# Kernel optimization log

Measured on AMD Instinct MI355X. Metric: run time of the kernel, lower is better.

## Reference

```python
import jax, jax.numpy as jnp
import numpy as np

B, N, C = 16, 2048, 128
NCLS = 40


def setup_inputs() -> dict:
    key = jax.random.key(0)
    ks = iter(jax.random.split(key, 40))

    def nrm(shape, s=0.05):
        return jax.random.normal(next(ks), shape, dtype=jnp.float32) * s

    return {
        "x": jax.random.normal(next(ks), (B, 3, N), dtype=jnp.float32),
        "conv1_w": nrm((128, 3), 0.5),
        "bn1_g": jnp.ones((128,), jnp.float32), "bn1_b": jnp.zeros((128,), jnp.float32),
        "conv2_w": nrm((128, 128)),
        "bn2_g": jnp.ones((128,), jnp.float32), "bn2_b": jnp.zeros((128,), jnp.float32),
        "sa_wqk": nrm((4, 32, 128)),
        "sa_wv": nrm((4, 128, 128)), "sa_bv": nrm((4, 128)),
        "sa_wt": nrm((4, 128, 128)), "sa_bt": nrm((4, 128)),
        "sa_g": jnp.ones((4, 128), jnp.float32), "sa_b": jnp.zeros((4, 128), jnp.float32),
        "fuse_w": nrm((1024, 512)),
        "fuse_g": jnp.ones((1024,), jnp.float32), "fuse_b": jnp.zeros((1024,), jnp.float32),
        "lin1_w": nrm((512, 1024)),
        "bn6_g": jnp.ones((512,), jnp.float32), "bn6_b": jnp.zeros((512,), jnp.float32),
        "lin2_w": nrm((256, 512)), "lin2_b": jnp.zeros((256,), jnp.float32),
        "bn7_g": jnp.ones((256,), jnp.float32), "bn7_b": jnp.zeros((256,), jnp.float32),
        "lin3_w": nrm((NCLS, 256)), "lin3_b": jnp.zeros((NCLS,), jnp.float32),
    }


def _pconv(w, x):
    # 1x1 Conv1d == channel matmul: [O,C] x [B,C,N] -> [B,O,N]
    return jnp.einsum('oc,bcn->bon', w, x)


def _fwd(x, conv1_w, bn1_g, bn1_b, conv2_w, bn2_g, bn2_b,
         sa_wqk, sa_wv, sa_bv, sa_wt, sa_bt, sa_g, sa_b,
         fuse_w, fuse_g, fuse_b, lin1_w, bn6_g, bn6_b,
         lin2_w, lin2_b, bn7_g, bn7_b, lin3_w, lin3_b):
    # conv stem (BN in eval mode: running mean=0, var=1 -> affine)
    h = jax.nn.relu(bn1_g[:, None] * _pconv(conv1_w, x) + bn1_b[:, None])
    h = jax.nn.relu(bn2_g[:, None] * _pconv(conv2_w, h) + bn2_b[:, None])

    outs = []
    for i in range(4):  # fixed number of structurally identical SA blocks
        # q_conv and k_conv share the same weight (aliased in the torch code)
        q = jnp.einsum('dc,bcn->bdn', sa_wqk[i], h)           # [B,32,N]
        energy = jnp.einsum('bdi,bdj->bij', q, q)             # [B,N,N]
        att = jax.nn.softmax(energy, axis=-1)
        att = att / (1e-9 + att.sum(axis=1, keepdims=True))   # extra L1 renorm over dim=1
        v = _pconv(sa_wv[i], h) + sa_bv[i][:, None]           # [B,C,N]
        x_r = jnp.einsum('bcn,bnm->bcm', v, att)              # [B,C,N]
        t = _pconv(sa_wt[i], h - x_r) + sa_bt[i][:, None]
        h = h + jax.nn.relu(sa_g[i][:, None] * t + sa_b[i][:, None])
        outs.append(h)

    cat = jnp.concatenate(outs, axis=1)                        # [B,512,N]
    f = fuse_g[:, None] * _pconv(fuse_w, cat) + fuse_b[:, None]
    f = jnp.where(f > 0, f, 0.2 * f)                           # LeakyReLU(0.2)
    g = f.max(axis=-1)                                         # adaptive max pool -> [B,1024]

    h1 = jax.nn.relu(bn6_g * (g @ lin1_w.T) + bn6_b)           # dropout = identity (eval)
    h2 = jax.nn.relu(bn7_g * (h1 @ lin2_w.T + lin2_b) + bn7_b)
    return h2 @ lin3_w.T + lin3_b                              # [B,40]


def reference(x, conv1_w, bn1_g, bn1_b, conv2_w, bn2_g, bn2_b,
              sa_wqk, sa_wv, sa_bv, sa_wt, sa_bt, sa_g, sa_b,
              fuse_w, fuse_g, fuse_b, lin1_w, bn6_g, bn6_b,
              lin2_w, lin2_b, bn7_g, bn7_b, lin3_w, lin3_b):
    return _fwd(x, conv1_w, bn1_g, bn1_b, conv2_w, bn2_g, bn2_b,
                sa_wqk, sa_wv, sa_bv, sa_wt, sa_bt, sa_g, sa_b,
                fuse_w, fuse_g, fuse_b, lin1_w, bn6_g, bn6_b,
                lin2_w, lin2_b, bn7_g, bn7_b, lin3_w, lin3_b)
```

## Files before the change

### kernel.cpp

```cpp
#include <hip/hip_runtime.h>

typedef __attribute__((ext_vector_type(4))) float f4;
typedef __attribute__((ext_vector_type(8))) short s16x8;
typedef __attribute__((ext_vector_type(4))) unsigned short us4;
typedef __attribute__((ext_vector_type(2))) unsigned int u32x2;
typedef unsigned short u16;
typedef unsigned int u32;

#define DEVI __device__ __forceinline__

DEVI u16 f2bf(float f){
    u32 u = __builtin_bit_cast(u32, f);
    u32 r = (u + 0x7fffu + ((u >> 16) & 1u)) >> 16;
    return (u16)r;
}
DEVI f4 mfma16(s16x8 a, s16x8 b, f4 c){
    return __builtin_amdgcn_mfma_f32_16x16x32_bf16(a, b, c, 0, 0, 0);
}
DEVI u32 cvtpk(float lo, float hi){
    u32 r;
    asm("v_cvt_pk_bf16_f32 %0, %1, %2" : "=v"(r) : "v"(lo), "v"(hi));
    return r;
}
DEVI void gload(const u16* g, u16* l){
    __builtin_amdgcn_global_load_lds((const __attribute__((address_space(1))) void*)g,
                                     (__attribute__((address_space(3))) void*)l, 16, 0, 0);
}

#define L2E 1.44269504088896340736f

__global__ __launch_bounds__(256) void k_cast(const float* w2, const float* wqk,
                                              const float* wv, const float* wt,
                                              const float* wf, u16* out){
    int i = blockIdx.x * 256 + threadIdx.x;
    if(i < 16384)       out[i] = f2bf(w2[i]);
    else if(i < 32768)  out[i] = f2bf(wqk[i - 16384]);
    else if(i < 98304)  out[i] = f2bf(wv[i - 32768]);
    else if(i < 163840) out[i] = f2bf(wt[i - 98304]);
    else if(i < 688128){
        int t = i - 163840;
        int o = t >> 9, c = t & 511;
        int jg = o >> 4, l15 = o & 15, ks = c >> 5, kr = c & 31;
        out[163840 + (size_t)(jg*16 + ks)*512 + l15*32 + kr] = f2bf(wf[t]);
    }
}

__global__ __launch_bounds__(256) void k_stem1(const float* x, const float* w1,
                                               const float* g1, const float* b1, u16* h1tb){
    int t = blockIdx.x * 256 + threadIdx.x;
    int b = t >> 11, n = t & 2047;
    const float* xb = x + (size_t)b * 3 * 2048 + n;
    float x0 = xb[0], x1 = xb[2048], x2 = xb[4096];
    u32* o = (u32*)(h1tb + (size_t)t * 128);
    #pragma unroll 8
    for(int c = 0; c < 128; c += 2){
        float a0 = fmaxf(g1[c]   * (w1[c*3+0]*x0 + w1[c*3+1]*x1 + w1[c*3+2]*x2) + b1[c],   0.f);
        float a1 = fmaxf(g1[c+1] * (w1[c*3+3]*x0 + w1[c*3+4]*x1 + w1[c*3+5]*x2) + b1[c+1], 0.f);
        o[c >> 1] = (u32)f2bf(a0) | ((u32)f2bf(a1) << 16);
    }
}

DEVI int swz512(int bid){ return ((bid & 7) << 6) | (bid >> 3); }
DEVI int swz1024(int bid){ return ((bid & 7) << 7) | (bid >> 3); }

DEVI void qv_phase(const u16* T, const u16* wqkb, const u16* wvb, const float* bv,
                   u16* qb, u16* vt, int b, int n0, int wv_, int l15, int kg){
    f4 accv[8], accq[2];
    #pragma unroll
    for(int j=0;j<8;j++) accv[j] = (f4){0.f,0.f,0.f,0.f};
    accq[0] = (f4){0.f,0.f,0.f,0.f}; accq[1] = accq[0];
    int row = wv_*16 + l15;
    #pragma unroll
    for(int ks=0; ks<4; ks++){
        s16x8 a = *(const s16x8*)&T[row*128 + ((ks*32 + kg*8) ^ ((row&7)<<3))];
        #pragma unroll
        for(int j=0;j<8;j++){
            s16x8 bb = *(const s16x8*)(wvb + (size_t)(j*16 + l15)*128 + ks*32 + kg*8);
            accv[j] = mfma16(a, bb, accv[j]);
        }
        #pragma unroll
        for(int f=0; f<2; f++){
            s16x8 wf_ = *(const s16x8*)(wqkb + (size_t)(f*16 + l15)*128 + ks*32 + kg*8);
            accq[f] = mfma16(wf_, a, accq[f]);
        }
    }
    int nb = n0 + wv_*16;
    int it = nb >> 5;
    int k0 = (nb & 31) + kg*4;
    int vbase = ((k0 >> 3)*16)*8 + (k0 & 7);
    #pragma unroll
    for(int j=0;j<8;j++){
        float bvo = bv[j*16 + l15];
        us4 pk;
        #pragma unroll
        for(int r=0;r<4;r++) pk[r] = f2bf(accv[j][r] + bvo);
        *(us4*)(vt + (size_t)((b*64 + it)*8 + j)*512 + vbase + l15*8) = pk;
    }
    int n = n0 + wv_*16 + l15;
    #pragma unroll
    for(int f=0; f<2; f++){
        us4 pk;
        #pragma unroll
        for(int r=0;r<4;r++) pk[r] = f2bf(accq[f][r]);
        *(us4*)(qb + (size_t)(b*2048 + n)*32 + f*16 + kg*4) = pk;
    }
}

__global__ __launch_bounds__(256) void k_conv2qv(const u16* h1tb, const u16* w2b,
                                                 const float* g2, const float* b2,
                                                 float* ht0,
                                                 const u16* wqkb, const u16* wvb,
                                                 const float* bv, u16* qb, u16* vt){
    __shared__ u16 T[8192];
    int bid2 = swz512(blockIdx.x);
    int b = bid2 >> 5;
    int n0 = (bid2 & 31) << 6;
    int lane = threadIdx.x & 63, wv_ = threadIdx.x >> 6;
    int l15 = lane & 15, kg = lane >> 4;
    const u16* arow = h1tb + (size_t)(b*2048 + n0 + wv_*16 + l15) * 128 + kg*8;
    f4 acc[8];
    #pragma unroll
    for(int j=0;j<8;j++) acc[j] = (f4){0.f,0.f,0.f,0.f};
    #pragma unroll
    for(int ks=0; ks<4; ks++){
        s16x8 a = *(const s16x8*)(arow + ks*32);
        #pragma unroll
        for(int j=0;j<8;j++){
            s16x8 bb = *(const s16x8*)(w2b + (size_t)(j*16 + l15)*128 + ks*32 + kg*8);
            acc[j] = mfma16(a, bb, acc[j]);
        }
    }
    int nn0 = n0 + wv_*16 + kg*4;
    #pragma unroll
    for(int j=0;j<8;j++){
        int o = j*16 + l15;
        float gg = g2[o], be = b2[o];
        #pragma unroll
        for(int r=0;r<4;r++){
            float h = fmaxf(gg * acc[j][r] + be, 0.f);
            int nl = wv_*16 + kg*4 + r;
            ht0[(size_t)(b*2048 + nn0 + r) * 128 + o] = h;
            T[nl*128 + (o ^ ((nl&7)<<3))] = f2bf(h);
        }
    }
    __syncthreads();
    qv_phase(T, wqkb, wvb, bv, qb, vt, b, n0, wv_, l15, kg);
}

__global__ __launch_bounds__(256) void k_passA(const u16* qb, float* crowp){
    int bid2 = swz1024(blockIdx.x);
    int b = bid2 >> 6;
    int rest = bid2 & 63;
    int i0 = (rest >> 1) << 6;
    int jh = rest & 1;
    int jbeg = jh << 10;
    int lane = threadIdx.x & 63, wv_ = threadIdx.x >> 6;
    int l15 = lane & 15, kg = lane >> 4;
    const u16* qbase = qb + (size_t)b * 2048 * 32;
    s16x8 af = *(const s16x8*)(qbase + (size_t)(i0 + wv_*16 + l15)*32 + kg*8);
    float m[4], s[4], mml[4];
    const f4 z = {0.f,0.f,0.f,0.f};
    {
        s16x8 b0 = *(const s16x8*)(qbase + (size_t)(jbeg + l15)*32 + kg*8);
        s16x8 b1 = *(const s16x8*)(qbase + (size_t)(jbeg + 16 + l15)*32 + kg*8);
        f4 e0 = mfma16(af, b0, z);
        f4 e1 = mfma16(af, b1, z);
        #pragma unroll
        for(int r=0;r<4;r++){
            m[r] = fmaxf(e0[r], e1[r]);
            mml[r] = -m[r]*L2E;
            s[r] = exp2f(fmaf(e0[r], L2E, mml[r])) + exp2f(fmaf(e1[r], L2E, mml[r]));
        }
    }
    for(int j0=jbeg+32; j0<jbeg+1024; j0+=32){
        s16x8 b0 = *(const s16x8*)(qbase + (size_t)(j0 + l15)*32 + kg*8);
        s16x8 b1 = *(const s16x8*)(qbase + (size_t)(j0 + 16 + l15)*32 + kg*8);
        f4 e0 = mfma16(af, b0, z);
        f4 e1 = mfma16(af, b1, z);
        #pragma unroll
        for(int r=0;r<4;r++){
            float mx = fmaxf(e0[r], e1[r]);
            if(mx > m[r] + 8.f){
                s[r] *= exp2f((m[r]-mx)*L2E);
                m[r] = mx; mml[r] = -mx*L2E;
            }
            s[r] += exp2f(fmaf(e0[r], L2E, mml[r])) + exp2f(fmaf(e1[r], L2E, mml[r]));
        }
    }
    #pragma unroll
    for(int d=1; d<16; d<<=1){
        #pragma unroll
        for(int r=0;r<4;r++){
            float mo = __shfl_xor(m[r], d);
            float so = __shfl_xor(s[r], d);
            float mn = fmaxf(m[r], mo);
            s[r] = s[r]*exp2f((m[r]-mn)*L2E) + so*exp2f((mo-mn)*L2E);
            m[r] = mn;
        }
    }
    if(l15 == 0){
        #pragma unroll
        for(int r=0;r<4;r++){
            int i = i0 + wv_*16 + kg*4 + r;
            crowp[jh*32768 + b*2048 + i] = m[r]*L2E + log2f(s[r]);
        }
    }
}

__global__ __launch_bounds__(256) void k_passB(const u16* qb, const u16* vt,
                                               const float* crowp,
                                               const float* hprev, int ldh,
                                               u16* dtb){
    __shared__ u16 V[2][8192];
    __shared__ u16 P[2][4096];
    __shared__ float CR[2048];
    __shared__ float csl[64];
    int bid2 = swz512(blockIdx.x);
    int b = bid2 >> 5;
    int j0 = (bid2 & 31) << 6;
    int tid = threadIdx.x;
    int lane = tid & 63, wv_ = tid >> 6;
    int l15 = lane & 15, kg = lane >> 4;
    int jh = wv_ * 16;
    const u16* qbase = qb + (size_t)b * 2048 * 32;
    const u16* vtb = vt + (size_t)b * 64*8*512;

    #pragma unroll
    for(int p=0;p<8;p++){
        int i = p*256 + tid;
        float c0 = crowp[b*2048 + i], c1 = crowp[32768 + b*2048 + i];
        float mx = fmaxf(c0, c1), mn = fminf(c0, c1);
        CR[i] = mx + log2f(1.f + exp2f(mn - mx));
    }

    s16x8 eb = *(const s16x8*)(qbase + (size_t)(j0 + jh + l15)*32 + kg*8);
    f4 acc[8];
    #pragma unroll
    for(int j=0;j<8;j++) acc[j] = (f4){0.f,0.f,0.f,0.f};
    float csp = 0.f;
    const f4 z = {0.f,0.f,0.f,0.f};

    auto stage = [&](int ic, int buf){
        const u16* src = vtb + (size_t)ic*8192 + wv_*2048 + lane*8;
        u16* dst = &V[buf][wv_*2048];
        #pragma unroll
        for(int p=0;p<4;p++) gload(src + p*512, dst + p*512);
    };
    auto eph = [&](int ic, int buf){
        #pragma unroll
        for(int isub=0; isub<4; isub++){
            s16x8 ea = *(const s16x8*)(qbase + (size_t)(ic*64 + isub*16 + l15)*32 + kg*8);
            f4 e = mfma16(ea, eb, z);
            f4 cc = *(const f4*)&CR[ic*64 + isub*16 + kg*4];
            float q0 = exp2f(fmaf(e[0], L2E, -cc[0]));
            float q1 = exp2f(fmaf(e[1], L2E, -cc[1]));
            float q2 = exp2f(fmaf(e[2], L2E, -cc[2]));
            float q3 = exp2f(fmaf(e[3], L2E, -cc[3]));
            csp += q0 + q1 + q2 + q3;
            u32x2 pk = { cvtpk(q0, q1), cvtpk(q2, q3) };
            int idx = wv_*1024 + (isub>>1)*512
                    + ((((isub&1)<<1) | (kg>>1))*16 + l15)*8 + (kg&1)*4;
            *(u32x2*)&P[buf][idx] = pk;
        }
    };

    __syncthreads();
    stage(0, 0);
    eph(0, 0);
    __syncthreads();
    for(int it=0; it<32; it++){
        int cur = it & 1;
        if(it < 31){ stage(it+1, cur^1); eph(it+1, cur^1); }
        s16x8 pa0 = *(const s16x8*)&P[cur][wv_*1024 + lane*8];
        s16x8 pa1 = *(const s16x8*)&P[cur][wv_*1024 + 512 + lane*8];
        __builtin_amdgcn_s_setprio(1);
        #pragma unroll
        for(int jc=0;jc<8;jc++){
            s16x8 vf = *(const s16x8*)&V[cur][jc*512 + lane*8];
            acc[jc] = mfma16(pa0, vf, acc[jc]);
        }
        #pragma unroll
        for(int jc=0;jc<8;jc++){
            s16x8 vf = *(const s16x8*)&V[cur][4096 + jc*512 + lane*8];
            acc[jc] = mfma16(pa1, vf, acc[jc]);
        }
        __builtin_amdgcn_s_setprio(0);
        __syncthreads();
    }
    csp += __shfl_xor(csp, 16);
    csp += __shfl_xor(csp, 32);
    if(lane < 16) csl[jh + l15] = csp;
    __syncthreads();
    #pragma unroll
    for(int r=0;r<4;r++){
        int jr = jh + kg*4 + r;
        float inv = 1.0f / (1e-9f + csl[jr]);
        int n = j0 + jr;
        const float* hrow = hprev + (size_t)(b*2048 + n)*ldh;
        u16* drow = dtb + (size_t)(b*2048 + n)*128;
        #pragma unroll
        for(int jc=0;jc<8;jc++){
            int c = jc*16 + l15;
            drow[c] = f2bf(hrow[c] - acc[jc][r]*inv);
        }
    }
}

__global__ __launch_bounds__(256) void k_tailqv(const u16* dtb, const u16* wtb, const float* bt,
                                                const float* sg, const float* sb,
                                                const float* hprev, int ldh,
                                                float* catf_o, u16* catb_o,
                                                const u16* wqkb, const u16* wvb,
                                                const float* bv, u16* qb, u16* vt, int doQV){
    __shared__ u16 T[8192];
    int bid2 = swz512(blockIdx.x);
    int b = bid2 >> 5;
    int n0 = (bid2 & 31) << 6;
    int lane = threadIdx.x & 63, wv_ = threadIdx.x >> 6;
    int l15 = lane & 15, kg = lane >> 4;
    const u16* arow = dtb + (size_t)(b*2048 + n0 + wv_*16 + l15) * 128 + kg*8;
    f4 acc[8];
    #pragma unroll
    for(int j=0;j<8;j++) acc[j] = (f4){0.f,0.f,0.f,0.f};
    #pragma unroll
    for(int ks=0; ks<4; ks++){
        s16x8 a = *(const s16x8*)(arow + ks*32);
        #pragma unroll
        for(int j=0;j<8;j++){
            s16x8 bb = *(const s16x8*)(wtb + (size_t)(j*16 + l15)*128 + ks*32 + kg*8);
            acc[j] = mfma16(a, bb, acc[j]);
        }
    }
    int nn0 = n0 + wv_*16 + kg*4;
    #pragma unroll
    for(int j=0;j<8;j++){
        int o = j*16 + l15;
        float bto = bt[o], gg = sg[o], be = sb[o];
        #pragma unroll
        for(int r=0;r<4;r++){
            int nn = nn0 + r;
            float t = acc[j][r] + bto;
            float hv = hprev[(size_t)(b*2048 + nn)*ldh + o];
            float hn = hv + fmaxf(gg*t + be, 0.f);
            size_t oi = (size_t)(b*2048 + nn)*512 + o;
            u16 hb = f2bf(hn);
            catf_o[oi] = hn;
            catb_o[oi] = hb;
            int nl = wv_*16 + kg*4 + r;
            T[nl*128 + (o ^ ((nl&7)<<3))] = hb;
        }
    }
    if(doQV){
        __syncthreads();
        qv_phase(T, wqkb, wvb, bv, qb, vt, b, n0, wv_, l15, kg);
    }
}

__global__ __launch_bounds__(512) void k_fuse(const u16* catb, const u16* wft,
                                              const float* fg, const float* fb, float* gpart){
    __shared__ u16 AB[24576];
    __shared__ float red[512];
    int bid2 = swz1024(blockIdx.x);
    int b  = bid2 >> 6;
    int rest = bid2 & 63;
    int ng = rest >> 2;
    int og = rest & 3;
    int tid = threadIdx.x;
    int lane = tid & 63, wv_ = tid >> 6;
    int wn = wv_ >> 2, wo = wv_ & 3;
    int l15 = lane & 15, kg = lane >> 4;

    f4 acc[4][4];
    #pragma unroll
    for(int mi=0;mi<4;mi++)
        #pragma unroll
        for(int j=0;j<4;j++) acc[mi][j] = (f4){0.f,0.f,0.f,0.f};

    for(int ksc=0; ksc<8; ksc++){
        if(ksc) __syncthreads();
        #pragma unroll
        for(int q=0;q<2;q++){
            int s = wv_*128 + q*64 + lane;
            int r = s >> 3;
            int c16 = (s & 7) ^ (r & 7);
            const u16* g = catb + (size_t)(b*2048 + ng*128 + r)*512 + ksc*64 + c16*8;
            gload(g, &AB[wv_*1024 + q*512]);
        }
        #pragma unroll
        for(int q=0;q<4;q++){
            int p = wv_*4 + q;
            int jgl = p >> 1, ksl = p & 1;
            const u16* g = wft + (size_t)((og*16 + jgl)*16 + ksc*2 + ksl)*512 + lane*8;
            gload(g, &AB[8192 + p*512]);
        }
        __syncthreads();
        #pragma unroll
        for(int ks=0; ks<2; ks++){
            s16x8 av[4], bw[4];
            #pragma unroll
            for(int mi=0;mi<4;mi++){
                int row = wn*64 + mi*16 + l15;
                av[mi] = *(const s16x8*)&AB[row*64 + ((ks*32 + kg*8) ^ ((row&7)<<3))];
            }
            #pragma unroll
            for(int j=0;j<4;j++){
                int p = (wo*4 + j)*2 + ks;
                bw[j] = *(const s16x8*)&AB[8192 + p*512 + l15*32 + kg*8];
            }
            #pragma unroll
            for(int j=0;j<4;j++)
                #pragma unroll
                for(int mi=0;mi<4;mi++)
                    acc[mi][j] = mfma16(av[mi], bw[j], acc[mi][j]);
        }
    }
    float vmax[4];
    #pragma unroll
    for(int j=0;j<4;j++){
        int o = og*256 + wo*64 + j*16 + l15;
        float fgv = fg[o], fbv = fb[o];
        float vm = -1e30f;
        #pragma unroll
        for(int mi=0;mi<4;mi++)
            #pragma unroll
            for(int r=0;r<4;r++){
                float f = fgv*acc[mi][j][r] + fbv;
                f = (f > 0.f) ? f : 0.2f*f;
                vm = fmaxf(vm, f);
            }
        vm = fmaxf(vm, __shfl_xor(vm, 16));
        vm = fmaxf(vm, __shfl_xor(vm, 32));
        vmax[j] = vm;
    }
    if(lane < 16){
        #pragma unroll
        for(int j=0;j<4;j++) red[(wo*2 + wn)*64 + j*16 + lane] = vmax[j];
    }
    __syncthreads();
    if(tid < 256){
        int wo2 = tid >> 6, ol = tid & 63;
        float m = fmaxf(red[(wo2*2+0)*64 + ol], red[(wo2*2+1)*64 + ol]);
        gpart[(size_t)(ng*16 + b)*1024 + og*256 + wo2*64 + ol] = m;
    }
}

__global__ __launch_bounds__(256) void k_gmax(const float* gpart, float* g){
    int i = blockIdx.x*256 + threadIdx.x;
    float m = gpart[i];
    #pragma unroll
    for(int p=1;p<16;p++) m = fmaxf(m, gpart[(size_t)p*16384 + i]);
    g[i] = m;
}

__global__ __launch_bounds__(256) void k_mlp(const float* in, const float* W, const float* bias,
                                             const float* gm, const float* bt, float* out,
                                             int IN, int OUT, int dorelu){
    int wid = blockIdx.x*4 + (threadIdx.x >> 6);
    int lane = threadIdx.x & 63;
    int b = wid / OUT, o = wid - b*OUT;
    if(b >= 16) return;
    const f4* ir = (const f4*)(in + (size_t)b*IN);
    const f4* wr = (const f4*)(W + (size_t)o*IN);
    float s = 0.f;
    for(int k=lane; k < (IN>>2); k += 64){
        f4 a = ir[k], w = wr[k];
        s += a[0]*w[0] + a[1]*w[1] + a[2]*w[2] + a[3]*w[3];
    }
    #pragma unroll
    for(int d=1; d<64; d<<=1) s += __shfl_xor(s, d);
    if(lane == 0){
        if(bias) s += bias[o];
        if(gm) s = gm[o]*s + bt[o];
        if(dorelu) s = fmaxf(s, 0.f);
        out[(size_t)b*OUT + o] = s;
    }
}

constexpr size_t OFF_WB   = 0;
constexpr size_t OFF_H1TB = 2u*1024*1024;
constexpr size_t OFF_HT0  = OFF_H1TB + 8388608;
constexpr size_t OFF_HTB0 = OFF_HT0 + 16777216;
constexpr size_t OFF_QB   = OFF_HTB0 + 8388608;
constexpr size_t OFF_VB   = OFF_QB + 2097152;
constexpr size_t OFF_CROW = OFF_VB + 8388608;
constexpr size_t OFF_GP   = OFF_CROW + 262144;
constexpr size_t OFF_DTB  = OFF_GP + 16777216 - 262144;
constexpr size_t OFF_CATF = OFF_DTB + 8388608;
constexpr size_t OFF_CATB = OFF_CATF + 67108864;
constexpr size_t OFF_G    = OFF_CATB + 33554432;
constexpr size_t OFF_H1V  = OFF_G + 65536;
constexpr size_t OFF_H2V  = OFF_H1V + 32768;

extern "C" void kernel_launch(void* const* d_in, const int* in_sizes, int n_in,
                              void* d_out, int out_size, void* d_ws, size_t ws_size,
                              hipStream_t stream){
    const float* x       = (const float*)d_in[0];
    const float* conv1_w = (const float*)d_in[1];
    const float* bn1_g   = (const float*)d_in[2];
    const float* bn1_b   = (const float*)d_in[3];
    const float* conv2_w = (const float*)d_in[4];
    const float* bn2_g   = (const float*)d_in[5];
    const float* bn2_b   = (const float*)d_in[6];
    const float* sa_wqk  = (const float*)d_in[7];
    const float* sa_wv   = (const float*)d_in[8];
    const float* sa_bv   = (const float*)d_in[9];
    const float* sa_wt   = (const float*)d_in[10];
    const float* sa_bt   = (const float*)d_in[11];
    const float* sa_g    = (const float*)d_in[12];
    const float* sa_b    = (const float*)d_in[13];
    const float* fuse_w  = (const float*)d_in[14];
    const float* fuse_g  = (const float*)d_in[15];
    const float* fuse_b  = (const float*)d_in[16];
    const float* lin1_w  = (const float*)d_in[17];
    const float* bn6_g   = (const float*)d_in[18];
    const float* bn6_b   = (const float*)d_in[19];
    const float* lin2_w  = (const float*)d_in[20];
    const float* lin2_b  = (const float*)d_in[21];
    const float* bn7_g   = (const float*)d_in[22];
    const float* bn7_b   = (const float*)d_in[23];
    const float* lin3_w  = (const float*)d_in[24];
    const float* lin3_b  = (const float*)d_in[25];

    char* ws = (char*)d_ws;
    u16*   wb    = (u16*)(ws + OFF_WB);
    u16*   h1tb  = (u16*)(ws + OFF_H1TB);
    float* ht0   = (float*)(ws + OFF_HT0);
    u16*   qbw   = (u16*)(ws + OFF_QB);
    u16*   vtw   = (u16*)(ws + OFF_VB);
    float* crowp = (float*)(ws + OFF_CROW);
    float* gpart = (float*)(ws + OFF_GP);
    u16*   dtb   = (u16*)(ws + OFF_DTB);
    float* catf  = (float*)(ws + OFF_CATF);
    u16*   catb  = (u16*)(ws + OFF_CATB);
    float* gbuf  = (float*)(ws + OFF_G);
    float* h1v   = (float*)(ws + OFF_H1V);
    float* h2v   = (float*)(ws + OFF_H2V);

    k_cast <<<2688, 256, 0, stream>>>(conv2_w, sa_wqk, sa_wv, sa_wt, fuse_w, wb);
    k_stem1<<<128,  256, 0, stream>>>(x, conv1_w, bn1_g, bn1_b, h1tb);
    k_conv2qv<<<512, 256, 0, stream>>>(h1tb, wb, bn2_g, bn2_b, ht0,
                                       wb + 16384, wb + 32768, sa_bv, qbw, vtw);

    for(int blk = 0; blk < 4; blk++){
        const float* hprev = (blk == 0) ? ht0 : (catf + (size_t)(blk-1)*128);
        int          ldh   = (blk == 0) ? 128 : 512;
        const u16* wtb  = wb + 98304 + blk*16384;
        int nb2 = (blk < 3) ? (blk + 1) : 3;
        const u16* wqkb2 = wb + 16384 + nb2*4096;
        const u16* wvb2  = wb + 32768 + nb2*16384;

        k_passA<<<1024, 256, 0, stream>>>(qbw, crowp);
        k_passB<<<512, 256, 0, stream>>>(qbw, vtw, crowp, hprev, ldh, dtb);
        k_tailqv<<<512, 256, 0, stream>>>(dtb, wtb, sa_bt + blk*128, sa_g + blk*128,
                                          sa_b + blk*128, hprev, ldh,
                                          catf + (size_t)blk*128, catb + (size_t)blk*128,
                                          wqkb2, wvb2, sa_bv + nb2*128, qbw, vtw,
                                          (blk < 3) ? 1 : 0);
    }

    k_fuse<<<1024, 512, 0, stream>>>(catb, wb + 163840, fuse_g, fuse_b, gpart);
    k_gmax<<<64,   256, 0, stream>>>(gpart, gbuf);
    k_mlp <<<2048, 256, 0, stream>>>(gbuf, lin1_w, nullptr, bn6_g, bn6_b, h1v, 1024, 512, 1);
    k_mlp <<<1024, 256, 0, stream>>>(h1v, lin2_w, lin2_b, bn7_g, bn7_b, h2v, 512, 256, 1);
    k_mlp <<<160,  256, 0, stream>>>(h2v, lin3_w, lin3_b, nullptr, nullptr,
                                     (float*)d_out, 256, 40, 0);
}
```

Before: 521.0 us.

## Split passB attention-V reduction across two wave halves with 512-thread blocks

Doubles the passB block to 512 threads. Each pair of waves splits the i-dimension (key) work of a 64-row tile in half, so each wave does half the exp/MFMA work per iteration. Partial accumulators and column sums are combined through shared memory (reusing the V buffer) before the final normalize-and-subtract store. This raises per-CU parallelism and latency hiding for a kernel with only 512 blocks, at the cost of an extra LDS reduction and more registers per CU.

```diff
diff --git a/kernel.cpp b/kernel.cpp
--- a/kernel.cpp
+++ b/kernel.cpp
@@ -207,27 +207,28 @@
     }
 }
 
-__global__ __launch_bounds__(256) void k_passB(const u16* qb, const u16* vt,
+__global__ __launch_bounds__(512) void k_passB(const u16* qb, const u16* vt,
                                                const float* crowp,
                                                const float* hprev, int ldh,
                                                u16* dtb){
     __shared__ u16 V[2][8192];
     __shared__ u16 P[2][4096];
     __shared__ float CR[2048];
-    __shared__ float csl[64];
+    __shared__ float csl[2][64];
     int bid2 = swz512(blockIdx.x);
     int b = bid2 >> 5;
     int j0 = (bid2 & 31) << 6;
     int tid = threadIdx.x;
     int lane = tid & 63, wv_ = tid >> 6;
+    int jw = wv_ >> 1, ih = wv_ & 1;
     int l15 = lane & 15, kg = lane >> 4;
-    int jh = wv_ * 16;
+    int jh = jw * 16;
     const u16* qbase = qb + (size_t)b * 2048 * 32;
     const u16* vtb = vt + (size_t)b * 64*8*512;
 
     #pragma unroll
-    for(int p=0;p<8;p++){
-        int i = p*256 + tid;
+    for(int p=0;p<4;p++){
+        int i = p*512 + tid;
         float c0 = crowp[b*2048 + i], c1 = crowp[32768 + b*2048 + i];
         float mx = fmaxf(c0, c1), mn = fminf(c0, c1);
         CR[i] = mx + log2f(1.f + exp2f(mn - mx));
@@ -241,14 +242,15 @@
     const f4 z = {0.f,0.f,0.f,0.f};
 
     auto stage = [&](int ic, int buf){
-        const u16* src = vtb + (size_t)ic*8192 + wv_*2048 + lane*8;
-        u16* dst = &V[buf][wv_*2048];
-        #pragma unroll
-        for(int p=0;p<4;p++) gload(src + p*512, dst + p*512);
+        const u16* src = vtb + (size_t)ic*8192 + wv_*1024 + lane*8;
+        u16* dst = &V[buf][wv_*1024];
+        gload(src, dst);
+        gload(src + 512, dst + 512);
     };
     auto eph = [&](int ic, int buf){
         #pragma unroll
-        for(int isub=0; isub<4; isub++){
+        for(int is=0; is<2; is++){
+            int isub = ih*2 + is;
             s16x8 ea = *(const s16x8*)(qbase + (size_t)(ic*64 + isub*16 + l15)*32 + kg*8);
             f4 e = mfma16(ea, eb, z);
             f4 cc = *(const f4*)&CR[ic*64 + isub*16 + kg*4];
@@ -258,8 +260,7 @@
             float q3 = exp2f(fmaf(e[3], L2E, -cc[3]));
             csp += q0 + q1 + q2 + q3;
             u32x2 pk = { cvtpk(q0, q1), cvtpk(q2, q3) };
-            int idx = wv_*1024 + (isub>>1)*512
-                    + ((((isub&1)<<1) | (kg>>1))*16 + l15)*8 + (kg&1)*4;
+            int idx = wv_*512 + ((is*2 + (kg>>1))*16 + l15)*8 + (kg&1)*4;
             *(u32x2*)&P[buf][idx] = pk;
         }
     };
@@ -271,37 +272,46 @@
     for(int it=0; it<32; it++){
         int cur = it & 1;
         if(it < 31){ stage(it+1, cur^1); eph(it+1, cur^1); }
-        s16x8 pa0 = *(const s16x8*)&P[cur][wv_*1024 + lane*8];
-        s16x8 pa1 = *(const s16x8*)&P[cur][wv_*1024 + 512 + lane*8];
+        s16x8 pa = *(const s16x8*)&P[cur][wv_*512 + lane*8];
         __builtin_amdgcn_s_setprio(1);
         #pragma unroll
         for(int jc=0;jc<8;jc++){
-            s16x8 vf = *(const s16x8*)&V[cur][jc*512 + lane*8];
-            acc[jc] = mfma16(pa0, vf, acc[jc]);
-        }
-        #pragma unroll
-        for(int jc=0;jc<8;jc++){
-            s16x8 vf = *(const s16x8*)&V[cur][4096 + jc*512 + lane*8];
-            acc[jc] = mfma16(pa1, vf, acc[jc]);
+            s16x8 vf = *(const s16x8*)&V[cur][ih*4096 + jc*512 + lane*8];
+            acc[jc] = mfma16(pa, vf, acc[jc]);
         }
         __builtin_amdgcn_s_setprio(0);
         __syncthreads();
     }
     csp += __shfl_xor(csp, 16);
     csp += __shfl_xor(csp, 32);
-    if(lane < 16) csl[jh + l15] = csp;
+    if(lane < 16) csl[ih][jh + l15] = csp;
     __syncthreads();
-    #pragma unroll
-    for(int r=0;r<4;r++){
-        int jr = jh + kg*4 + r;
-        float inv = 1.0f / (1e-9f + csl[jr]);
-        int n = j0 + jr;
-        const float* hrow = hprev + (size_t)(b*2048 + n)*ldh;
-        u16* drow = dtb + (size_t)(b*2048 + n)*128;
+    float* comb = (float*)V;
+    if(ih == 1){
+        #pragma unroll
+        for(int jc=0;jc<8;jc++)
+            *(f4*)&comb[jw*2048 + jc*256 + lane*4] = acc[jc];
+    }
+    __syncthreads();
+    if(ih == 0){
         #pragma unroll
         for(int jc=0;jc<8;jc++){
-            int c = jc*16 + l15;
-            drow[c] = f2bf(hrow[c] - acc[jc][r]*inv);
+            f4 o = *(const f4*)&comb[jw*2048 + jc*256 + lane*4];
+            acc[jc][0] += o[0]; acc[jc][1] += o[1];
+            acc[jc][2] += o[2]; acc[jc][3] += o[3];
+        }
+        #pragma unroll
+        for(int r=0;r<4;r++){
+            int jr = jh + kg*4 + r;
+            float inv = 1.0f / (1e-9f + csl[0][jr] + csl[1][jr]);
+            int n = j0 + jr;
+            const float* hrow = hprev + (size_t)(b*2048 + n)*ldh;
+            u16* drow = dtb + (size_t)(b*2048 + n)*128;
+            #pragma unroll
+            for(int jc=0;jc<8;jc++){
+                int c = jc*16 + l15;
+                drow[c] = f2bf(hrow[c] - acc[jc][r]*inv);
+            }
         }
     }
 }
@@ -550,7 +560,7 @@
         const u16* wvb2  = wb + 32768 + nb2*16384;
 
         k_passA<<<1024, 256, 0, stream>>>(qbw, crowp);
-        k_passB<<<512, 256, 0, stream>>>(qbw, vtw, crowp, hprev, ldh, dtb);
+        k_passB<<<512, 512, 0, stream>>>(qbw, vtw, crowp, hprev, ldh, dtb);
         k_tailqv<<<512, 256, 0, stream>>>(dtb, wtb, sa_bt + blk*128, sa_g + blk*128,
                                           sa_b + blk*128, hprev, ldh,
                                           catf + (size_t)blk*128, catb + (size_t)blk*128,
```

After: 494.8 us. 1.05x faster.
